# Kernel optimization log

Measured on AMD Instinct MI355X. Metric: run time of the kernel, lower is better.

The kernel has to match this reference:

```python
import jax, jax.numpy as jnp
import numpy as np

B, T, N, IN, OUT = 8, 48, 512, 256, 256
GR, NR = 16, 8
ALPHA = 1.0


def setup_inputs() -> dict:
    key = jax.random.key(0)
    ks = jax.random.split(key, 6)
    scale = 1.0 / np.sqrt(IN)
    x = jax.random.normal(ks[0], (B, T, N, IN), dtype=jnp.float32)
    W = jax.random.uniform(ks[1], (OUT, IN), jnp.float32, -scale, scale)
    b = jnp.zeros((OUT,), jnp.float32)
    gA = jax.random.uniform(ks[2], (IN, GR), jnp.float32, -scale, scale)
    gB = jax.random.uniform(ks[3], (GR, OUT), jnp.float32, -scale, scale) * 0.1
    nA = jax.random.uniform(ks[4], (N, IN, NR), jnp.float32, -scale, scale)
    nB = jax.random.uniform(ks[5], (N, NR, OUT), jnp.float32, -scale, scale) * 0.1
    return {"x": x, "W": W, "b": b, "gA": gA, "gB": gB, "nA": nA, "nB": nB}


def reference(x, W, b, gA, gB, nA, nB):
    # dense base: x @ W.T + b
    base = jnp.einsum('btni,oi->btno', x, W) + b
    # global LoRA: (x @ gA) @ gB * alpha/global_rank
    g = jnp.einsum('btnr,ro->btno', jnp.einsum('btni,ir->btnr', x, gA), gB) * (ALPHA / GR)
    # per-node LoRA
    p1 = jnp.einsum('btni,nir->btnr', x, nA)
    nd = jnp.einsum('btnr,nro->btno', p1, nB) * (ALPHA / NR)
    return base + g + nd
```

## Files before the change

### kernel.cpp

```cpp
#include <hip/hip_runtime.h>


typedef __attribute__((ext_vector_type(4))) float f32x4;
typedef __attribute__((ext_vector_type(8))) short short8;

__device__ __forceinline__ unsigned short f2bf(float f) {
    unsigned int u = __builtin_bit_cast(unsigned int, f);
    u += 0x7fffu + ((u >> 16) & 1u);
    return (unsigned short)(u >> 16);
}

__device__ __forceinline__ short8 cvt8(f32x4 a, f32x4 b) {
    short8 r;
    r[0] = (short)f2bf(a[0]); r[1] = (short)f2bf(a[1]);
    r[2] = (short)f2bf(a[2]); r[3] = (short)f2bf(a[3]);
    r[4] = (short)f2bf(b[0]); r[5] = (short)f2bf(b[1]);
    r[6] = (short)f2bf(b[2]); r[7] = (short)f2bf(b[3]);
    return r;
}

__global__ __launch_bounds__(512, 1) void fused_node_lora(
    const float* __restrict__ x, const float* __restrict__ W,
    const float* __restrict__ bias, const float* __restrict__ gA,
    const float* __restrict__ gB, const float* __restrict__ nA,
    const float* __restrict__ nB, float* __restrict__ out)
{
    extern __shared__ __align__(16) char smem[];
    const int n    = blockIdx.x;
    const int tid  = threadIdx.x;
    const int lane = tid & 63;
    const int w    = tid >> 6;
    const int l15  = lane & 15;
    const int kblk = lane >> 4;

    {
        short8 afr[2];
        #pragma unroll
        for (int t = 0; t < 2; ++t) {
            const int i = (w * 2 + t) * 16 + l15;
            const float* ap = (kblk == 2) ? (nA + ((long)n * 256 + i) * 8)
                                          : (gA + (long)i * 16 + (kblk & 1) * 8);
            const float sc = (kblk == 2) ? 0.125f : ((kblk == 3) ? 0.0f : 0.0625f);
            const float4 q0 = *(const float4*)(ap);
            const float4 q1 = *(const float4*)(ap + 4);
            short8 a;
            a[0] = (short)f2bf(q0.x * sc); a[1] = (short)f2bf(q0.y * sc);
            a[2] = (short)f2bf(q0.z * sc); a[3] = (short)f2bf(q0.w * sc);
            a[4] = (short)f2bf(q1.x * sc); a[5] = (short)f2bf(q1.y * sc);
            a[6] = (short)f2bf(q1.z * sc); a[7] = (short)f2bf(q1.w * sc);
            afr[t] = a;
        }
        for (int ot = 0; ot < 16; ++ot) {
            const int o = ot * 16 + l15;
            const float* bp = (kblk == 0) ? (gB + o)
                             : (kblk == 1) ? (gB + 2048 + o)
                                           : (nB + (long)n * 2048 + o);
            short8 bfr;
            #pragma unroll
            for (int j = 0; j < 8; ++j) bfr[j] = (short)f2bf(bp[j * 256]);
            const f32x4 zero = {0.f, 0.f, 0.f, 0.f};
            f32x4 c0 = __builtin_amdgcn_mfma_f32_16x16x32_bf16(afr[0], bfr, zero, 0, 0, 0);
            f32x4 c1 = __builtin_amdgcn_mfma_f32_16x16x32_bf16(afr[1], bfr, zero, 0, 0, 0);
            #pragma unroll
            for (int t = 0; t < 2; ++t) {
                const f32x4 c = t ? c1 : c0;
                const int ib = (w * 2 + t) * 16 + kblk * 4;
                const float4 wv = *(const float4*)(W + (long)o * 256 + ib);
                unsigned int lo = (unsigned int)f2bf(wv.x + c[0]) |
                                  ((unsigned int)f2bf(wv.y + c[1]) << 16);
                unsigned int hi = (unsigned int)f2bf(wv.z + c[2]) |
                                  ((unsigned int)f2bf(wv.w + c[3]) << 16);
                int byte = (o << 9) + (ib << 1);
                byte ^= ((o & 7) << 4);
                *reinterpret_cast<uint2*>(smem + byte) = make_uint2(lo, hi);
            }
        }
    }
    __syncthreads();

    const int wm = w & 3;
    const int wo = w >> 2;
    const long TSTR = 16L * 512 * 256;
    const float* xb = x + ((long)(wm * 96 + l15) * 512 + n) * 256 + kblk * 8;

    f32x4 buf[3][3][2];
    #define LDX(s2) do {                                                          \
        const int _p = (s2) >> 3, _k = (s2) & 7;                                  \
        _Pragma("unroll")                                                         \
        for (int _j = 0; _j < 3; ++_j) {                                          \
            const f32x4* _q = (const f32x4*)(xb + (long)(_p * 3 + _j) * TSTR + _k * 32); \
            buf[(s2) % 3][_j][0] = _q[0];                                         \
            buf[(s2) % 3][_j][1] = _q[1];                                         \
        } } while (0)

    LDX(0); LDX(1); LDX(2);

    #pragma unroll
    for (int p = 0; p < 2; ++p) {
        f32x4 acc[3][8];
        #pragma unroll
        for (int j = 0; j < 3; ++j)
            #pragma unroll
            for (int oi = 0; oi < 8; ++oi) { const f32x4 z = {0.f,0.f,0.f,0.f}; acc[j][oi] = z; }

        #pragma unroll
        for (int kt = 0; kt < 8; ++kt) {
            const int s = p * 8 + kt;
            short8 af[3];
            #pragma unroll
            for (int j = 0; j < 3; ++j) af[j] = cvt8(buf[s % 3][j][0], buf[s % 3][j][1]);
            if (s + 3 < 16) LDX(s + 3);
            const unsigned int kaddr =
                ((((unsigned)l15 << 9) | ((unsigned)kt << 6) | ((unsigned)kblk << 4))
                 ^ (((unsigned)(l15 & 7)) << 4));
            #pragma unroll
            for (int oi = 0; oi < 8; ++oi) {
                const short8 bf = *reinterpret_cast<const short8*>(
                    smem + kaddr + (unsigned)(wo * 8 + oi) * 8192u);
                #pragma unroll
                for (int j = 0; j < 3; ++j)
                    acc[j][oi] = __builtin_amdgcn_mfma_f32_16x16x32_bf16(bf, af[j], acc[j][oi], 0, 0, 0);
            }
        }

        #pragma unroll
        for (int oi = 0; oi < 8; ++oi) {
            const int ot = wo * 8 + oi;
            const f32x4 bv = *(const f32x4*)(bias + ot * 16 + kblk * 4);
            #pragma unroll
            for (int j = 0; j < 3; ++j) {
                f32x4 v = acc[j][oi];
                v[0] += bv[0]; v[1] += bv[1]; v[2] += bv[2]; v[3] += bv[3];
                float* ob = out + ((long)((wm * 6 + p * 3 + j) * 16 + l15) * 512 + n) * 256
                            + ot * 16 + kblk * 4;
                __builtin_nontemporal_store(v, (f32x4*)ob);
            }
        }
    }
    #undef LDX
}

extern "C" void kernel_launch(void* const* d_in, const int* in_sizes, int n_in,
                              void* d_out, int out_size, void* d_ws, size_t ws_size,
                              hipStream_t stream) {
    const float* x  = (const float*)d_in[0];
    const float* W  = (const float*)d_in[1];
    const float* b  = (const float*)d_in[2];
    const float* gA = (const float*)d_in[3];
    const float* gB = (const float*)d_in[4];
    const float* nA = (const float*)d_in[5];
    const float* nB = (const float*)d_in[6];
    float* out = (float*)d_out;
    (void)hipFuncSetAttribute((const void*)fused_node_lora,
                              hipFuncAttributeMaxDynamicSharedMemorySize, 131072);
    fused_node_lora<<<dim3(512), dim3(512), 131072, stream>>>(x, W, b, gA, gB, nA, nB, out);
}
```

Before: 107.9 us.

## Split output columns across two blocks per node and prefetch x earlier

Each node is now handled by two blocks, each owning half of the 256 output columns. This halves the shared-memory weight tile to 64KB and doubles the grid to 1024 blocks, with launch bounds raised to allow more resident blocks. The x prefetch is moved ahead of the per-node weight construction so global loads overlap that setup, and the buffering depth drops from three stages to two. The cost is that both halves re-read x and recompute the LoRA low-rank products, so x traffic from HBM/L2 doubles unless the paired blocks share it in cache.

```diff
diff --git a/kernel.cpp b/kernel.cpp
--- a/kernel.cpp
+++ b/kernel.cpp
@@ -19,26 +19,45 @@
     return r;
 }
 
-__global__ __launch_bounds__(512, 1) void fused_node_lora(
+__global__ __launch_bounds__(512, 4) void fused_node_lora(
     const float* __restrict__ x, const float* __restrict__ W,
     const float* __restrict__ bias, const float* __restrict__ gA,
     const float* __restrict__ gB, const float* __restrict__ nA,
     const float* __restrict__ nB, float* __restrict__ out)
 {
     extern __shared__ __align__(16) char smem[];
-    const int n    = blockIdx.x;
+    const int bid  = blockIdx.x;
+    const int node = ((bid >> 4) << 3) | (bid & 7);
+    const int half = (bid >> 3) & 1;
     const int tid  = threadIdx.x;
     const int lane = tid & 63;
     const int w    = tid >> 6;
     const int l15  = lane & 15;
     const int kblk = lane >> 4;
 
+    const int wm = w & 3;
+    const int wo = w >> 2;
+    const long TSTR = 16L * 512 * 256;
+    const float* xb = x + ((long)(wm * 96 + l15) * 512 + node) * 256 + kblk * 8;
+
+    f32x4 buf[2][3][2];
+    #define LDX(s2) do {                                                          \
+        const int _p = (s2) >> 3, _k = (s2) & 7;                                  \
+        _Pragma("unroll")                                                         \
+        for (int _j = 0; _j < 3; ++_j) {                                          \
+            const f32x4* _q = (const f32x4*)(xb + (long)(_p * 3 + _j) * TSTR + _k * 32); \
+            buf[(s2) & 1][_j][0] = _q[0];                                         \
+            buf[(s2) & 1][_j][1] = _q[1];                                         \
+        } } while (0)
+
+    LDX(0); LDX(1);
+
     {
         short8 afr[2];
         #pragma unroll
         for (int t = 0; t < 2; ++t) {
             const int i = (w * 2 + t) * 16 + l15;
-            const float* ap = (kblk == 2) ? (nA + ((long)n * 256 + i) * 8)
+            const float* ap = (kblk == 2) ? (nA + ((long)node * 256 + i) * 8)
                                           : (gA + (long)i * 16 + (kblk & 1) * 8);
             const float sc = (kblk == 2) ? 0.125f : ((kblk == 3) ? 0.0f : 0.0625f);
             const float4 q0 = *(const float4*)(ap);
@@ -50,11 +69,12 @@
             a[6] = (short)f2bf(q1.z * sc); a[7] = (short)f2bf(q1.w * sc);
             afr[t] = a;
         }
-        for (int ot = 0; ot < 16; ++ot) {
-            const int o = ot * 16 + l15;
+        for (int ot = 0; ot < 8; ++ot) {
+            const int ol = ot * 16 + l15;
+            const int o  = half * 128 + ol;
             const float* bp = (kblk == 0) ? (gB + o)
                              : (kblk == 1) ? (gB + 2048 + o)
-                                           : (nB + (long)n * 2048 + o);
+                                           : (nB + (long)node * 2048 + o);
             short8 bfr;
             #pragma unroll
             for (int j = 0; j < 8; ++j) bfr[j] = (short)f2bf(bp[j * 256]);
@@ -70,53 +90,36 @@
                                   ((unsigned int)f2bf(wv.y + c[1]) << 16);
                 unsigned int hi = (unsigned int)f2bf(wv.z + c[2]) |
                                   ((unsigned int)f2bf(wv.w + c[3]) << 16);
-                int byte = (o << 9) + (ib << 1);
-                byte ^= ((o & 7) << 4);
+                int byte = (ol << 9) + (ib << 1);
+                byte ^= ((ol & 7) << 4);
                 *reinterpret_cast<uint2*>(smem + byte) = make_uint2(lo, hi);
             }
         }
     }
     __syncthreads();
 
-    const int wm = w & 3;
-    const int wo = w >> 2;
-    const long TSTR = 16L * 512 * 256;
-    const float* xb = x + ((long)(wm * 96 + l15) * 512 + n) * 256 + kblk * 8;
-
-    f32x4 buf[3][3][2];
-    #define LDX(s2) do {                                                          \
-        const int _p = (s2) >> 3, _k = (s2) & 7;                                  \
-        _Pragma("unroll")                                                         \
-        for (int _j = 0; _j < 3; ++_j) {                                          \
-            const f32x4* _q = (const f32x4*)(xb + (long)(_p * 3 + _j) * TSTR + _k * 32); \
-            buf[(s2) % 3][_j][0] = _q[0];                                         \
-            buf[(s2) % 3][_j][1] = _q[1];                                         \
-        } } while (0)
-
-    LDX(0); LDX(1); LDX(2);
-
     #pragma unroll
     for (int p = 0; p < 2; ++p) {
-        f32x4 acc[3][8];
+        f32x4 acc[3][4];
         #pragma unroll
         for (int j = 0; j < 3; ++j)
             #pragma unroll
-            for (int oi = 0; oi < 8; ++oi) { const f32x4 z = {0.f,0.f,0.f,0.f}; acc[j][oi] = z; }
+            for (int oi = 0; oi < 4; ++oi) { const f32x4 z = {0.f,0.f,0.f,0.f}; acc[j][oi] = z; }
 
         #pragma unroll
         for (int kt = 0; kt < 8; ++kt) {
             const int s = p * 8 + kt;
             short8 af[3];
             #pragma unroll
-            for (int j = 0; j < 3; ++j) af[j] = cvt8(buf[s % 3][j][0], buf[s % 3][j][1]);
-            if (s + 3 < 16) LDX(s + 3);
+            for (int j = 0; j < 3; ++j) af[j] = cvt8(buf[s & 1][j][0], buf[s & 1][j][1]);
+            if (s + 2 < 16) LDX(s + 2);
             const unsigned int kaddr =
                 ((((unsigned)l15 << 9) | ((unsigned)kt << 6) | ((unsigned)kblk << 4))
                  ^ (((unsigned)(l15 & 7)) << 4));
             #pragma unroll
-            for (int oi = 0; oi < 8; ++oi) {
+            for (int oi = 0; oi < 4; ++oi) {
                 const short8 bf = *reinterpret_cast<const short8*>(
-                    smem + kaddr + (unsigned)(wo * 8 + oi) * 8192u);
+                    smem + kaddr + (unsigned)(wo * 4 + oi) * 8192u);
                 #pragma unroll
                 for (int j = 0; j < 3; ++j)
                     acc[j][oi] = __builtin_amdgcn_mfma_f32_16x16x32_bf16(bf, af[j], acc[j][oi], 0, 0, 0);
@@ -124,15 +127,14 @@
         }
 
         #pragma unroll
-        for (int oi = 0; oi < 8; ++oi) {
-            const int ot = wo * 8 + oi;
-            const f32x4 bv = *(const f32x4*)(bias + ot * 16 + kblk * 4);
+        for (int oi = 0; oi < 4; ++oi) {
+            const int oc = half * 128 + (wo * 4 + oi) * 16 + kblk * 4;
+            const f32x4 bv = *(const f32x4*)(bias + oc);
             #pragma unroll
             for (int j = 0; j < 3; ++j) {
                 f32x4 v = acc[j][oi];
                 v[0] += bv[0]; v[1] += bv[1]; v[2] += bv[2]; v[3] += bv[3];
-                float* ob = out + ((long)((wm * 6 + p * 3 + j) * 16 + l15) * 512 + n) * 256
-                            + ot * 16 + kblk * 4;
+                float* ob = out + ((long)((wm * 6 + p * 3 + j) * 16 + l15) * 512 + node) * 256 + oc;
                 __builtin_nontemporal_store(v, (f32x4*)ob);
             }
         }
@@ -152,6 +154,6 @@
     const float* nB = (const float*)d_in[6];
     float* out = (float*)d_out;
     (void)hipFuncSetAttribute((const void*)fused_node_lora,
-                              hipFuncAttributeMaxDynamicSharedMemorySize, 131072);
-    fused_node_lora<<<dim3(512), dim3(512), 131072, stream>>>(x, W, b, gA, gB, nA, nB, out);
+                              hipFuncAttributeMaxDynamicSharedMemorySize, 65536);
+    fused_node_lora<<<dim3(1024), dim3(512), 65536, stream>>>(x, W, b, gA, gB, nA, nB, out);
 }
```

New measurement: 147.5 us. +36.8%, slower.
